# Performance work log

Measured on AMD Instinct MI355X. Metric: run time of the kernel, lower is better.

## Reference

```python
import jax, jax.numpy as jnp
import numpy as np
from jax import lax

N_EMBD = 1024
N_HEAD = 16
HEAD_DIM = N_EMBD // N_HEAD
EPS = 1e-6
B, T = 4, 2048


def setup_inputs() -> dict:
    key = jax.random.key(0)
    ks = jax.random.split(key, 5)
    scale = 1.0 / np.sqrt(N_EMBD)
    return {
        "x": jax.random.normal(ks[0], (B, T, N_EMBD), jnp.float32),
        "W_attn": jax.random.normal(ks[1], (N_EMBD, 3 * N_EMBD), jnp.float32) * scale,
        "b_attn": jax.random.normal(ks[2], (3 * N_EMBD,), jnp.float32) * 0.01,
        "W_proj": jax.random.normal(ks[3], (N_EMBD, N_EMBD), jnp.float32) * scale,
        "b_proj": jax.random.normal(ks[4], (N_EMBD,), jnp.float32) * 0.01,
    }


def _feature_map(x):
    # ELU + 1 for non-negativity
    return jax.nn.elu(x) + 1.0


def reference(x, W_attn, b_attn, W_proj, b_proj):
    Bb, Tt, C = x.shape
    qkv = x @ W_attn + b_attn  # (B,T,3C)
    q, k, v = jnp.split(qkv, 3, axis=-1)

    def to_heads(t):
        # (B,T,C) -> (T,B,H,d): scan axis leading
        return t.reshape(Bb, Tt, N_HEAD, HEAD_DIM).transpose(1, 0, 2, 3)

    q = _feature_map(to_heads(q))
    k = _feature_map(to_heads(k))
    v = to_heads(v)

    # Causal linear attention: O(d^2) running state instead of the torch
    # code's materialized (B,H,T,d,d) cumsum — same math.
    def step(carry, inp):
        kv, ksum = carry  # (B,H,d,d), (B,H,d)
        qt, kt, vt = inp  # each (B,H,d)
        kv = kv + kt[..., :, None] * vt[..., None, :]
        ksum = ksum + kt
        num = jnp.einsum('bhi,bhij->bhj', qt, kv)
        den = jnp.einsum('bhi,bhi->bh', qt, ksum)[..., None] + EPS
        return (kv, ksum), num / den

    init = (
        jnp.zeros((Bb, N_HEAD, HEAD_DIM, HEAD_DIM), x.dtype),
        jnp.zeros((Bb, N_HEAD, HEAD_DIM), x.dtype),
    )
    _, y = lax.scan(step, init, (q, k, v))  # (T,B,H,d)
    y = y.transpose(1, 0, 2, 3).reshape(Bb, Tt, C)
    return y @ W_proj + b_proj  # dropout is identity in eval mode
```

## Files before the change

kernel.cpp:

```cpp
#include <hip/hip_runtime.h>
#include <math.h>

#define BB   4
#define TT   2048
#define CC   1024
#define HH   16
#define DD   64
#define MM   (BB*TT)
#define NQKV (3*CC)
#define LCH  128
#define NCH  (TT/LCH)
#define EPSF 1e-6f

#define PST  136
#define VTST 136

typedef __bf16 bf16x8 __attribute__((ext_vector_type(8)));
typedef float  floatx4 __attribute__((ext_vector_type(4)));

__device__ __forceinline__ unsigned short f2bf(float f) {
  union { float f; unsigned int u; } v; v.f = f;
  unsigned int r = v.u + 0x7fffu + ((v.u >> 16) & 1u);
  return (unsigned short)(r >> 16);
}
__device__ __forceinline__ float bf2f(unsigned short s) {
  union { unsigned int u; float f; } v; v.u = ((unsigned int)s) << 16;
  return v.f;
}
__device__ __forceinline__ float featmap(float v) {
  return v > 0.f ? v + 1.f : __expf(v);
}
__device__ __forceinline__ void gld_lds_b128(const unsigned short* g, unsigned short* l) {
  __builtin_amdgcn_global_load_lds(
      (const __attribute__((address_space(1))) unsigned int*)g,
      (__attribute__((address_space(3))) unsigned int*)l, 16, 0, 0);
}

__device__ __forceinline__ void transpose_cvt_body(const float* __restrict__ W,
                                                   unsigned short* __restrict__ out,
                                                   int R, int Cc, int bx32, int by32, int tid) {
  __shared__ float tile[32][33];
  int tx = tid & 31, ty = tid >> 5;
  int bx = bx32 * 32, by = by32 * 32;
  #pragma unroll
  for (int i = ty; i < 32; i += 8)
    tile[i][tx] = W[(size_t)(by + i) * Cc + bx + tx];
  __syncthreads();
  #pragma unroll
  for (int i = ty; i < 32; i += 8)
    out[(size_t)(bx + i) * R + by + tx] = f2bf(tile[tx][i]);
}

__global__ __launch_bounds__(256) void prep_kernel(
    const float* __restrict__ x, unsigned short* __restrict__ xb,
    const float* __restrict__ Wa, unsigned short* __restrict__ WaT,
    const float* __restrict__ Wp, unsigned short* __restrict__ WpT) {
  int blk = blockIdx.x, tid = threadIdx.x;
  if (blk < 8192) {
    int i = (blk * 256 + tid) * 4;
    float4 f = *(const float4*)(x + i);
    ushort4 o;
    o.x = f2bf(f.x); o.y = f2bf(f.y); o.z = f2bf(f.z); o.w = f2bf(f.w);
    *(ushort4*)(xb + i) = o;
  } else if (blk < 8192 + 3072) {
    int t = blk - 8192;
    transpose_cvt_body(Wa, WaT, CC, NQKV, t % 96, t / 96, tid);
  } else {
    int t = blk - 11264;
    transpose_cvt_body(Wp, WpT, CC, CC, t % 32, t / 32, tid);
  }
}

#define BKQ   32
#define ASLT  (256 * BKQ)
#define BSLT  (192 * BKQ)
#define NT_Q  (CC / BKQ)

__global__ __launch_bounds__(512, 2) void gemm_qkv_kernel(
    const unsigned short* __restrict__ A, const unsigned short* __restrict__ Bt,
    const float* __restrict__ bias,
    unsigned short* __restrict__ qh, unsigned short* __restrict__ kh,
    unsigned short* __restrict__ vh) {
  extern __shared__ __align__(16) unsigned short lds[];
  unsigned short* Ar = lds;
  unsigned short* Br = lds + 4 * ASLT;

  const int tid = threadIdx.x;
  const int wave = tid >> 6, lane = tid & 63;
  const int lr = lane & 15, lq = lane >> 4;
  const int lin = blockIdx.y * 16 + blockIdx.x;
  const int lin2 = (lin & 7) * 64 + (lin >> 3);
  const int m0 = (lin2 >> 4) * 256, n0 = (lin2 & 15) * 192;
  const int wm = (wave >> 2) * 128, wn = (wave & 3) * 48;

  const int srow = wave * 16 + (lane >> 2);
  const int cs = (lane & 3) ^ ((lane >> 3) & 3);
  const unsigned short* gA0 = A  + (size_t)(m0 + srow) * CC + cs * 8;
  const unsigned short* gB0 = Bt + (size_t)(n0 + srow) * CC + cs * 8;
  unsigned short* const stA = Ar + wave * 512;
  unsigned short* const stB = Br + wave * 512;
  const bool bhi = (wave < 4);

  const int chunk = lq ^ ((lr >> 1) & 3);
  const int roA = (wm + lr) * BKQ + chunk * 8;
  const int roB = (wn + lr) * BKQ + chunk * 8;

  floatx4 acc[3][8] = {};

#define QSTAGE_A(tt) do {                                      \
    const unsigned short* g_ = gA0 + (tt) * BKQ;               \
    unsigned short* d_ = stA + ((tt) & 3) * ASLT;              \
    gld_lds_b128(g_, d_);                                      \
    gld_lds_b128(g_ + (size_t)128 * CC, d_ + 4096);            \
  } while (0)
#define QSTAGE_B(tt) do {                                      \
    const unsigned short* g_ = gB0 + (tt) * BKQ;               \
    unsigned short* d_ = stB + ((tt) & 3) * BSLT;              \
    gld_lds_b128(g_, d_);                                      \
    if (bhi) gld_lds_b128(g_ + (size_t)128 * CC, d_ + 4096);   \
  } while (0)

  QSTAGE_A(0); QSTAGE_B(0);
  QSTAGE_A(1); QSTAGE_B(1);
  QSTAGE_A(2); QSTAGE_B(2);
  asm volatile("s_waitcnt vmcnt(6)" ::: "memory");
  __builtin_amdgcn_s_barrier();

  #pragma unroll 4
  for (int t = 0; t < NT_Q; ++t) {
    const unsigned short* sA = Ar + (t & 3) * ASLT + roA;
    const unsigned short* sB = Br + (t & 3) * BSLT + roB;
    bf16x8 an[3], bm[8];
    #pragma unroll
    for (int i = 0; i < 3; i++) an[i] = *(const bf16x8*)(sB + i * (16 * BKQ));
    #pragma unroll
    for (int j = 0; j < 8; j++) bm[j] = *(const bf16x8*)(sA + j * (16 * BKQ));
    if (t < NT_Q - 3) { QSTAGE_A(t + 3); QSTAGE_B(t + 3); }
    __builtin_amdgcn_s_barrier();
    asm volatile("s_waitcnt lgkmcnt(0)" ::: "memory");
    __builtin_amdgcn_s_setprio(1);
    #pragma unroll
    for (int i = 0; i < 3; i++)
      #pragma unroll
      for (int j = 0; j < 8; j++)
        acc[i][j] = __builtin_amdgcn_mfma_f32_16x16x32_bf16(an[i], bm[j], acc[i][j], 0, 0, 0);
    __builtin_amdgcn_s_setprio(0);
    if (t < NT_Q - 3)        asm volatile("s_waitcnt vmcnt(6)" ::: "memory");
    else if (t == NT_Q - 3)  asm volatile("s_waitcnt vmcnt(3)" ::: "memory");
    else if (t == NT_Q - 2)  asm volatile("s_waitcnt vmcnt(0)" ::: "memory");
    __builtin_amdgcn_s_barrier();
  }
#undef QSTAGE_A
#undef QSTAGE_B

  unsigned short* dstv[3];
  size_t qoff[3];
  float4 bi[3];
  bool feat[3];
  #pragma unroll
  for (int i = 0; i < 3; i++) {
    const int n = n0 + wn + i * 16 + lq * 4;
    dstv[i] = (n < 1024) ? qh : (n < 2048) ? kh : vh;
    feat[i] = (n < 2048);
    const int h = (n & 1023) >> 6, dd = n & 63;
    qoff[i] = (size_t)h * (TT * DD) + dd;
    bi[i] = *(const float4*)&bias[n];
  }
  #pragma unroll
  for (int j = 0; j < 8; j++) {
    const int m = m0 + wm + j * 16 + lr;
    const int b = m >> 11, tg = m & 2047;
    const size_t pj = (size_t)b * (HH * TT * DD) + (size_t)tg * DD;
    #pragma unroll
    for (int i = 0; i < 3; i++) {
      float v0 = acc[i][j][0] + bi[i].x, v1 = acc[i][j][1] + bi[i].y;
      float v2 = acc[i][j][2] + bi[i].z, v3 = acc[i][j][3] + bi[i].w;
      if (feat[i]) { v0 = featmap(v0); v1 = featmap(v1); v2 = featmap(v2); v3 = featmap(v3); }
      ushort4 o; o.x = f2bf(v0); o.y = f2bf(v1); o.z = f2bf(v2); o.w = f2bf(v3);
      *(ushort4*)&dstv[i][pj + qoff[i]] = o;
    }
  }
}

#define PBK   32
#define PASLT (128 * PBK)
#define PBSLT (256 * PBK)
#define NT_P  (CC / PBK)

__global__ __launch_bounds__(512, 2) void gemm_proj_kernel(
    const unsigned short* __restrict__ A, const unsigned short* __restrict__ Bt,
    const float* __restrict__ bias, float* __restrict__ out) {
  extern __shared__ __align__(16) unsigned short lds[];
  unsigned short* Ar = lds;
  unsigned short* Br = lds + 4 * PASLT;

  const int tid = threadIdx.x;
  const int wave = tid >> 6, lane = tid & 63;
  const int lr = lane & 15, lq = lane >> 4;
  const int lin = blockIdx.y * 4 + blockIdx.x;
  const int lin2 = (lin & 7) * 32 + (lin >> 3);
  const int m0 = (lin2 >> 2) * 128, n0 = (lin2 & 3) * 256;
  const int wm = (wave >> 2) * 64, wn = (wave & 3) * 64;

  const int srow = wave * 16 + (lane >> 2);
  const int cs = (lane & 3) ^ ((lane >> 3) & 3);
  const unsigned short* gA0 = A  + (size_t)(m0 + srow) * CC + cs * 8;
  const unsigned short* gB0 = Bt + (size_t)(n0 + srow) * CC + cs * 8;
  unsigned short* const stA = Ar + wave * 512;
  unsigned short* const stB = Br + wave * 512;

  const int chunk = lq ^ ((lr >> 1) & 3);
  const int roA = (wm + lr) * PBK + chunk * 8;
  const int roB = (wn + lr) * PBK + chunk * 8;

  floatx4 acc[4][4] = {};

#define PSTAGE(tt) do {                                        \
    const unsigned short* ga_ = gA0 + (tt) * PBK;              \
    unsigned short* da_ = stA + ((tt) & 3) * PASLT;            \
    gld_lds_b128(ga_, da_);                                    \
    const unsigned short* gb_ = gB0 + (tt) * PBK;              \
    unsigned short* db_ = stB + ((tt) & 3) * PBSLT;            \
    gld_lds_b128(gb_, db_);                                    \
    gld_lds_b128(gb_ + (size_t)128 * CC, db_ + 4096);          \
  } while (0)

  PSTAGE(0); PSTAGE(1); PSTAGE(2);
  asm volatile("s_waitcnt vmcnt(6)" ::: "memory");
  __builtin_amdgcn_s_barrier();

  #pragma unroll 4
  for (int t = 0; t < NT_P; ++t) {
    const unsigned short* sA = Ar + (t & 3) * PASLT + roA;
    const unsigned short* sB = Br + (t & 3) * PBSLT + roB;
    bf16x8 an[4], bm[4];
    #pragma unroll
    for (int i = 0; i < 4; i++) an[i] = *(const bf16x8*)(sB + i * (16 * PBK));
    #pragma unroll
    for (int j = 0; j < 4; j++) bm[j] = *(const bf16x8*)(sA + j * (16 * PBK));
    if (t < NT_P - 3) PSTAGE(t + 3);
    __builtin_amdgcn_s_barrier();
    asm volatile("s_waitcnt lgkmcnt(0)" ::: "memory");
    __builtin_amdgcn_s_setprio(1);
    #pragma unroll
    for (int i = 0; i < 4; i++)
      #pragma unroll
      for (int j = 0; j < 4; j++)
        acc[i][j] = __builtin_amdgcn_mfma_f32_16x16x32_bf16(an[i], bm[j], acc[i][j], 0, 0, 0);
    __builtin_amdgcn_s_setprio(0);
    if (t < NT_P - 3)        asm volatile("s_waitcnt vmcnt(6)" ::: "memory");
    else if (t == NT_P - 3)  asm volatile("s_waitcnt vmcnt(3)" ::: "memory");
    else if (t == NT_P - 2)  asm volatile("s_waitcnt vmcnt(0)" ::: "memory");
    __builtin_amdgcn_s_barrier();
  }
#undef PSTAGE

  #pragma unroll
  for (int i = 0; i < 4; i++) {
    const int n = n0 + wn + i * 16 + lq * 4;
    const float4 bi = *(const float4*)&bias[n];
    #pragma unroll
    for (int j = 0; j < 4; j++) {
      const int m = m0 + wm + j * 16 + lr;
      float4 o;
      o.x = acc[i][j][0] + bi.x; o.y = acc[i][j][1] + bi.y;
      o.z = acc[i][j][2] + bi.z; o.w = acc[i][j][3] + bi.w;
      *(float4*)&out[(size_t)m * CC + n] = o;
    }
  }
}

__global__ __launch_bounds__(256) void chunk_state_kernel(
    const unsigned short* __restrict__ kh, const unsigned short* __restrict__ vh,
    float* __restrict__ KVx) {
  __shared__ __align__(16) unsigned short Kt[64 * VTST];
  __shared__ __align__(16) unsigned short Vt[80 * VTST];
  int blk = blockIdx.x;
  int bh = blk / NCH, c = blk % NCH;
  int tid = threadIdx.x;
  const unsigned short* kp = kh + ((size_t)bh * TT + c * LCH) * DD;
  const unsigned short* vp = vh + ((size_t)bh * TT + c * LCH) * DD;
  {
    int t = tid & 127, j0 = (tid >> 7) * 8;
    union { uint4 u; unsigned short s[8]; } wk[4], wv[4];
    #pragma unroll
    for (int ii = 0; ii < 4; ii++) {
      wk[ii].u = *(const uint4*)&kp[(size_t)t * DD + j0 + ii * 16];
      wv[ii].u = *(const uint4*)&vp[(size_t)t * DD + j0 + ii * 16];
    }
    #pragma unroll
    for (int ii = 0; ii < 4; ii++) {
      const int j8 = j0 + ii * 16;
      #pragma unroll
      for (int jj = 0; jj < 8; jj++) {
        Kt[(j8 + jj) * VTST + t] = wk[ii].s[jj];
        Vt[(j8 + jj) * VTST + t] = wv[ii].s[jj];
      }
    }
  }
  for (int e = tid; e < 16 * 128; e += 256) {
    int rr = e >> 7, n = e & 127;
    Vt[(64 + rr) * VTST + n] = (rr == 0) ? (unsigned short)0x3F80 : (unsigned short)0;
  }
  __syncthreads();
  int wave = tid >> 6, lane = tid & 63;
  int lr = lane & 15, lq = lane >> 4;
  int i0 = wave * 16;
  floatx4 acc[5] = {};
  #pragma unroll
  for (int kk = 0; kk < 4; kk++) {
    bf16x8 a = *(const bf16x8*)&Kt[(i0 + lr) * VTST + kk * 32 + lq * 8];
    #pragma unroll
    for (int jt = 0; jt < 5; jt++) {
      bf16x8 b = *(const bf16x8*)&Vt[(jt * 16 + lr) * VTST + kk * 32 + lq * 8];
      acc[jt] = __builtin_amdgcn_mfma_f32_16x16x32_bf16(a, b, acc[jt], 0, 0, 0);
    }
  }
  float* o = KVx + (size_t)blk * 5120;
  #pragma unroll
  for (int jt = 0; jt < 5; jt++)
    *(float4*)&o[(jt * 16 + lr) * 64 + i0 + lq * 4] = *(float4*)&acc[jt];
}

__global__ __launch_bounds__(256) void prefix_state_kernel(const float* __restrict__ KVx,
                                                           unsigned short* __restrict__ SPb) {
  int bh = blockIdx.x / 5, jb = blockIdx.x % 5;
  int e = jb * 1024 + threadIdx.x * 4;
  size_t base0 = ((size_t)bh * NCH) * 5120 + e;
  float4 v[NCH];
  #pragma unroll
  for (int c = 0; c < NCH; c++)
    v[c] = *(const float4*)&KVx[base0 + (size_t)c * 5120];
  float r0 = 0.f, r1 = 0.f, r2 = 0.f, r3 = 0.f;
  #pragma unroll
  for (int c = 0; c < NCH; c++) {
    ushort4 o;
    o.x = f2bf(r0); o.y = f2bf(r1); o.z = f2bf(r2); o.w = f2bf(r3);
    *(ushort4*)&SPb[base0 + (size_t)c * 5120] = o;
    r0 += v[c].x; r1 += v[c].y; r2 += v[c].z; r3 += v[c].w;
  }
}

__global__ __launch_bounds__(256) void chunk_attn_kernel(
    const unsigned short* __restrict__ qh, const unsigned short* __restrict__ kh,
    const unsigned short* __restrict__ vh, const unsigned short* __restrict__ SPb,
    unsigned short* __restrict__ yb) {
  __shared__ __align__(16) unsigned short lds[17408 + 80 * VTST];
  unsigned short* Qs = lds;
  unsigned short* Ks = lds + 8192;
  unsigned short* P  = lds;
  unsigned short* Vt = lds + 17408;

  int blk = blockIdx.x;
  int bh = blk / NCH, c = blk % NCH;
  int b = bh / HH, h = bh % HH;
  int tid = threadIdx.x;
  const unsigned short* qp = qh + ((size_t)bh * TT + c * LCH) * DD;
  const unsigned short* kp = kh + ((size_t)bh * TT + c * LCH) * DD;
  const unsigned short* vp = vh + ((size_t)bh * TT + c * LCH) * DD;

  int wave = tid >> 6, lane = tid & 63;
  int lr = lane & 15, lq = lane >> 4;
  int mbase = wave * 32;

  const int vt = tid & 127, vj0 = (tid >> 7) * 8;
  uint4 wv[4];
  #pragma unroll
  for (int ii = 0; ii < 4; ii++)
    wv[ii] = *(const uint4*)&vp[(size_t)vt * DD + vj0 + ii * 16];
  asm volatile("" ::: "memory");

  {
    const int grow8 = lane >> 3;
    const int gc = (lane & 7) ^ grow8;
    const unsigned short* gq = qp + (size_t)(wave * 32 + grow8) * DD + gc * 8;
    const unsigned short* gk = kp + (size_t)(wave * 32 + grow8) * DD + gc * 8;
    unsigned short* dq = Qs + wave * 32 * DD;
    unsigned short* dk = Ks + wave * 32 * DD;
    #pragma unroll
    for (int g = 0; g < 4; g++) {
      gld_lds_b128(gq + (size_t)g * 8 * DD, dq + g * 512);
      gld_lds_b128(gk + (size_t)g * 8 * DD, dk + g * 512);
    }
  }

  #pragma unroll
  for (int ii = 0; ii < 4; ii++) {
    union { uint4 u; unsigned short s[8]; } w; w.u = wv[ii];
    const int j8 = vj0 + ii * 16;
    #pragma unroll
    for (int jj = 0; jj < 8; jj++) Vt[(j8 + jj) * VTST + vt] = w.s[jj];
  }
  for (int e = tid; e < 16 * 128; e += 256) {
    int rr = e >> 7, n = e & 127;
    Vt[(64 + rr) * VTST + n] = (rr == 0) ? (unsigned short)0x3F80 : (unsigned short)0;
  }
  asm volatile("s_waitcnt vmcnt(0)" ::: "memory");
  __syncthreads();

  bf16x8 aq[2][2];
  #pragma unroll
  for (int i = 0; i < 2; i++)
    #pragma unroll
    for (int kk = 0; kk < 2; kk++)
      aq[i][kk] = *(const bf16x8*)&Qs[(mbase + i * 16 + lr) * DD +
                                      ((((kk << 2) + lq) ^ (lr & 7)) << 3)];

  floatx4 accT[5][2] = {};
  const unsigned short* spb = SPb + (size_t)blk * (80 * 64);
  #pragma unroll
  for (int jt = 0; jt < 5; jt++)
    #pragma unroll
    for (int kk = 0; kk < 2; kk++) {
      bf16x8 asp = *(const bf16x8*)&spb[(jt * 16 + lr) * 64 + kk * 32 + lq * 8];
      accT[jt][0] = __builtin_amdgcn_mfma_f32_16x16x32_bf16(asp, aq[0][kk], accT[jt][0], 0, 0, 0);
      accT[jt][1] = __builtin_amdgcn_mfma_f32_16x16x32_bf16(asp, aq[1][kk], accT[jt][1], 0, 0, 0);
    }
  floatx4 sacc[2][8] = {};
  #pragma unroll
  for (int nt = 0; nt < 8; nt++)
    #pragma unroll
    for (int kk = 0; kk < 2; kk++) {
      bf16x8 bk = *(const bf16x8*)&Ks[(nt * 16 + lr) * DD +
                                      ((((kk << 2) + lq) ^ (lr & 7)) << 3)];
      sacc[0][nt] = __builtin_amdgcn_mfma_f32_16x16x32_bf16(aq[0][kk], bk, sacc[0][nt], 0, 0, 0);
      sacc[1][nt] = __builtin_amdgcn_mfma_f32_16x16x32_bf16(aq[1][kk], bk, sacc[1][nt], 0, 0, 0);
    }
  __syncthreads();

  #pragma unroll
  for (int i = 0; i < 2; i++)
    #pragma unroll
    for (int nt = 0; nt < 8; nt++) {
      int col = nt * 16 + lr;
      #pragma unroll
      for (int r = 0; r < 4; r++) {
        int m = mbase + i * 16 + lq * 4 + r;
        float v = (col <= m) ? sacc[i][nt][r] : 0.f;
        P[m * PST + col] = f2bf(v);
      }
    }
  __syncthreads();

  #pragma unroll
  for (int kk4 = 0; kk4 < 4; kk4++) {
    bf16x8 bp0 = *(const bf16x8*)&P[(mbase + lr) * PST + kk4 * 32 + lq * 8];
    bf16x8 bp1 = *(const bf16x8*)&P[(mbase + 16 + lr) * PST + kk4 * 32 + lq * 8];
    #pragma unroll
    for (int jt = 0; jt < 5; jt++) {
      bf16x8 av = *(const bf16x8*)&Vt[(jt * 16 + lr) * VTST + kk4 * 32 + lq * 8];
      accT[jt][0] = __builtin_amdgcn_mfma_f32_16x16x32_bf16(av, bp0, accT[jt][0], 0, 0, 0);
      accT[jt][1] = __builtin_amdgcn_mfma_f32_16x16x32_bf16(av, bp1, accT[jt][1], 0, 0, 0);
    }
  }

  #pragma unroll
  for (int it = 0; it < 2; it++) {
    float den = __shfl(accT[4][it][0], lr, 64);
    float inv = 1.f / (den + EPSF);
    int tg = c * LCH + mbase + it * 16 + lr;
    size_t base = ((size_t)b * TT + tg) * CC + h * DD;
    #pragma unroll
    for (int jt = 0; jt < 4; jt++) {
      ushort4 o;
      o.x = f2bf(accT[jt][it][0] * inv);
      o.y = f2bf(accT[jt][it][1] * inv);
      o.z = f2bf(accT[jt][it][2] * inv);
      o.w = f2bf(accT[jt][it][3] * inv);
      *(ushort4*)&yb[base + jt * 16 + lq * 4] = o;
    }
  }
}

extern "C" void kernel_launch(void* const* d_in, const int* in_sizes, int n_in,
                              void* d_out, int out_size, void* d_ws, size_t ws_size,
                              hipStream_t stream) {
  const float* x      = (const float*)d_in[0];
  const float* W_attn = (const float*)d_in[1];
  const float* b_attn = (const float*)d_in[2];
  const float* W_proj = (const float*)d_in[3];
  const float* b_proj = (const float*)d_in[4];
  float* out = (float*)d_out;

  char* ws = (char*)d_ws;
  size_t off = 0;
  auto alloc = [&](size_t bytes) -> char* {
    char* p = ws + off;
    off += (bytes + 255) & ~(size_t)255;
    return p;
  };
  unsigned short* xb  = (unsigned short*)alloc((size_t)MM * CC * 2);
  unsigned short* WaT = (unsigned short*)alloc((size_t)NQKV * CC * 2);
  unsigned short* WpT = (unsigned short*)alloc((size_t)CC * CC * 2);
  unsigned short* qh  = (unsigned short*)alloc((size_t)MM * CC * 2);
  unsigned short* kh  = (unsigned short*)alloc((size_t)MM * CC * 2);
  unsigned short* vh  = (unsigned short*)alloc((size_t)MM * CC * 2);
  float* KVx = (float*)alloc((size_t)BB * HH * NCH * 80 * 64 * 4);
  unsigned short* SPb = (unsigned short*)alloc((size_t)BB * HH * NCH * 80 * 64 * 2);
  unsigned short* yb = xb;

  static bool s_attr_done = false;
  if (!s_attr_done) {
    (void)hipFuncSetAttribute((const void*)gemm_qkv_kernel,
                              hipFuncAttributeMaxDynamicSharedMemorySize, 114688);
    (void)hipFuncSetAttribute((const void*)gemm_proj_kernel,
                              hipFuncAttributeMaxDynamicSharedMemorySize, 98304);
    s_attr_done = true;
  }

  prep_kernel<<<12288, 256, 0, stream>>>(x, xb, W_attn, WaT, W_proj, WpT);
  gemm_qkv_kernel<<<dim3(NQKV / 192, MM / 256), 512, 114688, stream>>>(xb, WaT, b_attn, qh, kh, vh);
  chunk_state_kernel<<<BB * HH * NCH, 256, 0, stream>>>(kh, vh, KVx);
  prefix_state_kernel<<<BB * HH * 5, 256, 0, stream>>>(KVx, SPb);
  chunk_attn_kernel<<<BB * HH * NCH, 256, 0, stream>>>(qh, kh, vh, SPb, yb);
  gemm_proj_kernel<<<dim3(CC / 256, MM / 128), 512, 98304, stream>>>(yb, WpT, b_proj, out);
}
```

Before: 217.0 us.

## Fuse prefix-state scan into chunk_state via last-block atomic counter

The separate prefix_state kernel launch is removed. Each chunk_state block now bumps a per-(batch,head) atomic counter, and the last block to finish for that head computes the exclusive prefix sum over the chunk states and writes SPb. The counter is reset in prep_kernel. Separately, chunk_attn now loads its SPb fragments into registers early so that load latency overlaps with the Q/K staging. The trade-off is that the scan runs serially in one block per head (5 groups per block) instead of across 320 blocks, and it adds fence and atomic overhead.

```diff
diff --git a/kernel.cpp b/kernel.cpp
--- a/kernel.cpp
+++ b/kernel.cpp
@@ -54,8 +54,10 @@
 __global__ __launch_bounds__(256) void prep_kernel(
     const float* __restrict__ x, unsigned short* __restrict__ xb,
     const float* __restrict__ Wa, unsigned short* __restrict__ WaT,
-    const float* __restrict__ Wp, unsigned short* __restrict__ WpT) {
+    const float* __restrict__ Wp, unsigned short* __restrict__ WpT,
+    unsigned int* __restrict__ cnt) {
   int blk = blockIdx.x, tid = threadIdx.x;
+  if (blk == 0 && tid < BB * HH) cnt[tid] = 0;
   if (blk < 8192) {
     int i = (blk * 256 + tid) * 4;
     float4 f = *(const float4*)(x + i);
@@ -272,7 +274,8 @@
 
 __global__ __launch_bounds__(256) void chunk_state_kernel(
     const unsigned short* __restrict__ kh, const unsigned short* __restrict__ vh,
-    float* __restrict__ KVx) {
+    float* __restrict__ KVx, unsigned short* __restrict__ SPb,
+    unsigned int* __restrict__ cnt) {
   __shared__ __align__(16) unsigned short Kt[64 * VTST];
   __shared__ __align__(16) unsigned short Vt[80 * VTST];
   int blk = blockIdx.x;
@@ -320,24 +323,31 @@
   #pragma unroll
   for (int jt = 0; jt < 5; jt++)
     *(float4*)&o[(jt * 16 + lr) * 64 + i0 + lq * 4] = *(float4*)&acc[jt];
-}
-
-__global__ __launch_bounds__(256) void prefix_state_kernel(const float* __restrict__ KVx,
-                                                           unsigned short* __restrict__ SPb) {
-  int bh = blockIdx.x / 5, jb = blockIdx.x % 5;
-  int e = jb * 1024 + threadIdx.x * 4;
-  size_t base0 = ((size_t)bh * NCH) * 5120 + e;
-  float4 v[NCH];
-  #pragma unroll
-  for (int c = 0; c < NCH; c++)
-    v[c] = *(const float4*)&KVx[base0 + (size_t)c * 5120];
-  float r0 = 0.f, r1 = 0.f, r2 = 0.f, r3 = 0.f;
-  #pragma unroll
-  for (int c = 0; c < NCH; c++) {
-    ushort4 o;
-    o.x = f2bf(r0); o.y = f2bf(r1); o.z = f2bf(r2); o.w = f2bf(r3);
-    *(ushort4*)&SPb[base0 + (size_t)c * 5120] = o;
-    r0 += v[c].x; r1 += v[c].y; r2 += v[c].z; r3 += v[c].w;
+
+  __threadfence();
+  __shared__ unsigned int s_old;
+  __syncthreads();
+  if (tid == 0) s_old = atomicAdd(&cnt[bh], 1u);
+  __syncthreads();
+  if (s_old == NCH - 1) {
+    __threadfence();
+    const size_t b0 = (size_t)bh * NCH * 5120;
+    #pragma unroll
+    for (int g = 0; g < 5; g++) {
+      const int e = g * 1024 + tid * 4;
+      float4 v[NCH];
+      #pragma unroll
+      for (int c2 = 0; c2 < NCH; c2++)
+        v[c2] = *(const float4*)&KVx[b0 + (size_t)c2 * 5120 + e];
+      float r0 = 0.f, r1 = 0.f, r2 = 0.f, r3 = 0.f;
+      #pragma unroll
+      for (int c2 = 0; c2 < NCH; c2++) {
+        ushort4 ob;
+        ob.x = f2bf(r0); ob.y = f2bf(r1); ob.z = f2bf(r2); ob.w = f2bf(r3);
+        *(ushort4*)&SPb[b0 + (size_t)c2 * 5120 + e] = ob;
+        r0 += v[c2].x; r1 += v[c2].y; r2 += v[c2].z; r3 += v[c2].w;
+      }
+    }
   }
 }
 
@@ -368,6 +378,13 @@
   #pragma unroll
   for (int ii = 0; ii < 4; ii++)
     wv[ii] = *(const uint4*)&vp[(size_t)vt * DD + vj0 + ii * 16];
+  const unsigned short* spb = SPb + (size_t)blk * (80 * 64);
+  bf16x8 aspr[5][2];
+  #pragma unroll
+  for (int jt = 0; jt < 5; jt++)
+    #pragma unroll
+    for (int kk = 0; kk < 2; kk++)
+      aspr[jt][kk] = *(const bf16x8*)&spb[(jt * 16 + lr) * 64 + kk * 32 + lq * 8];
   asm volatile("" ::: "memory");
 
   {
@@ -407,14 +424,12 @@
                                       ((((kk << 2) + lq) ^ (lr & 7)) << 3)];
 
   floatx4 accT[5][2] = {};
-  const unsigned short* spb = SPb + (size_t)blk * (80 * 64);
   #pragma unroll
   for (int jt = 0; jt < 5; jt++)
     #pragma unroll
     for (int kk = 0; kk < 2; kk++) {
-      bf16x8 asp = *(const bf16x8*)&spb[(jt * 16 + lr) * 64 + kk * 32 + lq * 8];
-      accT[jt][0] = __builtin_amdgcn_mfma_f32_16x16x32_bf16(asp, aq[0][kk], accT[jt][0], 0, 0, 0);
-      accT[jt][1] = __builtin_amdgcn_mfma_f32_16x16x32_bf16(asp, aq[1][kk], accT[jt][1], 0, 0, 0);
+      accT[jt][0] = __builtin_amdgcn_mfma_f32_16x16x32_bf16(aspr[jt][kk], aq[0][kk], accT[jt][0], 0, 0, 0);
+      accT[jt][1] = __builtin_amdgcn_mfma_f32_16x16x32_bf16(aspr[jt][kk], aq[1][kk], accT[jt][1], 0, 0, 0);
     }
   floatx4 sacc[2][8] = {};
   #pragma unroll
@@ -497,6 +512,7 @@
   unsigned short* vh  = (unsigned short*)alloc((size_t)MM * CC * 2);
   float* KVx = (float*)alloc((size_t)BB * HH * NCH * 80 * 64 * 4);
   unsigned short* SPb = (unsigned short*)alloc((size_t)BB * HH * NCH * 80 * 64 * 2);
+  unsigned int* cnt = (unsigned int*)alloc(BB * HH * sizeof(unsigned int));
   unsigned short* yb = xb;
 
   static bool s_attr_done = false;
@@ -508,10 +524,9 @@
     s_attr_done = true;
   }
 
-  prep_kernel<<<12288, 256, 0, stream>>>(x, xb, W_attn, WaT, W_proj, WpT);
+  prep_kernel<<<12288, 256, 0, stream>>>(x, xb, W_attn, WaT, W_proj, WpT, cnt);
   gemm_qkv_kernel<<<dim3(NQKV / 192, MM / 256), 512, 114688, stream>>>(xb, WaT, b_attn, qh, kh, vh);
-  chunk_state_kernel<<<BB * HH * NCH, 256, 0, stream>>>(kh, vh, KVx);
-  prefix_state_kernel<<<BB * HH * 5, 256, 0, stream>>>(KVx, SPb);
+  chunk_state_kernel<<<BB * HH * NCH, 256, 0, stream>>>(kh, vh, KVx, SPb, cnt);
   chunk_attn_kernel<<<BB * HH * NCH, 256, 0, stream>>>(qh, kh, vh, SPb, yb);
   gemm_proj_kernel<<<dim3(CC / 256, MM / 128), 512, 98304, stream>>>(yb, WpT, b_proj, out);
 }
```

Result: slower. 381.5 us (+75.8%).
